# Performance work log

Hardware: AMD Instinct MI355X
Metric: run time of the kernel (lower is better)

Reference implementation:

```python
import jax, jax.numpy as jnp
import numpy as np

B, N = 1, 512
NODE_DIM, EDGE_DIM = 384, 128
H, SK, SV, PK, PV = 8, 16, 16, 4, 4
EPS = 1e-8
LN_EPS = 1e-5


def setup_inputs() -> dict:
    key = jax.random.key(0)
    ks = jax.random.split(key, 20)
    d, e = NODE_DIM, EDGE_DIM
    s = 0.02
    rn = lambda k, sh: jax.random.normal(k, sh, jnp.float32) * s
    # orthonormal per-residue rotations (valid rigid frames)
    R, _ = jnp.linalg.qr(jax.random.normal(ks[2], (B, N, 3, 3), jnp.float32))
    out_dim = H * (SV + EDGE_DIM + PV * 4)  # scalar + pairwise + points(3) + point norms(1)
    return dict(
        node_features=jax.random.normal(ks[0], (B, N, d), jnp.float32),
        edge_features=jax.random.normal(ks[1], (B, N, N, e), jnp.float32),
        rotations=R,
        translations=jax.random.normal(ks[3], (B, N, 3), jnp.float32),
        mask=jnp.ones((B, N), bool),
        Wq_s=rn(ks[4], (d, H * SK)), Wk_s=rn(ks[5], (d, H * SK)), Wv_s=rn(ks[6], (d, H * SV)),
        Wq_p=rn(ks[7], (d, H * PK * 3)), Wk_p=rn(ks[8], (d, H * PK * 3)), Wv_p=rn(ks[9], (d, H * PV * 3)),
        point_weights=jnp.full((H,), np.log(np.e - 1.0), jnp.float32),  # softplus -> 1
        Wb=rn(ks[10], (e, H)), bb=jnp.zeros((H,), jnp.float32),
        Wo=rn(ks[11], (out_dim, d)), bo=jnp.zeros((d,), jnp.float32),
        g1=jnp.ones((d,), jnp.float32), beta1=jnp.zeros((d,), jnp.float32),
        W1=rn(ks[12], (d, 2 * d)), b1=jnp.zeros((2 * d,), jnp.float32),
        W2=rn(ks[13], (2 * d, 2 * d)), b2=jnp.zeros((2 * d,), jnp.float32),
        W3=rn(ks[14], (2 * d, d)), b3=jnp.zeros((d,), jnp.float32),
        g2=jnp.ones((d,), jnp.float32), beta2=jnp.zeros((d,), jnp.float32),
    )


def _layer_norm(x, g, b):
    mu = x.mean(-1, keepdims=True)
    var = ((x - mu) ** 2).mean(-1, keepdims=True)
    return (x - mu) * jax.lax.rsqrt(var + LN_EPS) * g + b


def _forward(node_features, edge_features, rotations, translations, mask,
             Wq_s, Wk_s, Wv_s, Wq_p, Wk_p, Wv_p, point_weights, Wb, bb, Wo, bo,
             g1, beta1, W1, b1, W2, b2, W3, b3, g2, beta2):
    b, n, d = node_features.shape
    # num_attn_logits = 3 (scalar + point + pairwise)
    scal_scale = (3 * SK) ** -0.5
    point_scale = (3 * PK * 4.5) ** -0.5
    pair_scale = 3 ** -0.5

    qs = (node_features @ Wq_s).reshape(b, n, H, SK)
    kk = (node_features @ Wk_s).reshape(b, n, H, SK)
    vs = (node_features @ Wv_s).reshape(b, n, H, SV)

    def apply_rigid(p):  # p: (b,n,h,d,3); global = R^T applied per lucidrains einsum + t
        return jnp.einsum('bnhdc,bncr->bnhdr', p, rotations) + translations[:, :, None, None, :]

    qp = apply_rigid((node_features @ Wq_p).reshape(b, n, H, PK, 3))
    kp = apply_rigid((node_features @ Wk_p).reshape(b, n, H, PK, 3))
    vp = apply_rigid((node_features @ Wv_p).reshape(b, n, H, PV, 3))

    logits = jnp.einsum('bihk,bjhk->bhij', qs, kk) * scal_scale

    # point distance term: sum_{d,c} (q-k)^2 = |q|^2 + |k|^2 - 2 q.k (avoids (b,h,i,j,d,3) tensor)
    w = jax.nn.softplus(point_weights)  # (H,)
    q2 = jnp.einsum('bnhdc,bnhdc->bhn', qp, qp)
    k2 = jnp.einsum('bnhdc,bnhdc->bhn', kp, kp)
    cross = jnp.einsum('bihdc,bjhdc->bhij', qp, kp)
    dist = q2[..., :, None] + k2[..., None, :] - 2.0 * cross  # (b,h,i,j)
    logits = logits - 0.5 * point_scale * w[None, :, None, None] * dist

    pair_bias = (jnp.einsum('bije,eh->bhij', edge_features, Wb) + bb[None, :, None, None]) * pair_scale
    logits = logits + pair_bias

    pm = mask[:, None, :, None] & mask[:, None, None, :]  # (b,1,i,j)
    logits = jnp.where(pm, logits, -jnp.finfo(logits.dtype).max)
    attn = jax.nn.softmax(logits, axis=-1)  # (b,h,i,j)

    rs = jnp.einsum('bhij,bjhv->bihv', attn, vs).reshape(b, n, H * SV)
    rp = jnp.einsum('bhij,bije->bihe', attn, edge_features).reshape(b, n, H * EDGE_DIM)
    pts = jnp.einsum('bhij,bjhdc->bihdc', attn, vp)
    # invert rigid: subtract t, apply R (inverse of R^T application)
    local = jnp.einsum('bihdc,birc->bihdr', pts - translations[:, :, None, None, :], rotations)
    norms = jnp.sqrt((local ** 2).sum(-1) + EPS)  # (b,n,H,PV)

    cat = jnp.concatenate([rs, local.reshape(b, n, H * PV * 3), norms.reshape(b, n, H * PV), rp], axis=-1)
    ipa_out = cat @ Wo + bo

    x = _layer_norm(ipa_out, g1, beta1)  # dropout is identity at eval
    x = jax.nn.relu(x @ W1 + b1)
    x = jax.nn.relu(x @ W2 + b2)
    x = x @ W3 + b3
    return _layer_norm(x, g2, beta2)


def reference(node_features, edge_features, rotations, translations, mask,
              Wq_s, Wk_s, Wv_s, Wq_p, Wk_p, Wv_p, point_weights, Wb, bb, Wo, bo,
              g1, beta1, W1, b1, W2, b2, W3, b3, g2, beta2):
    return _forward(node_features, edge_features, rotations, translations, mask,
                    Wq_s, Wk_s, Wv_s, Wq_p, Wk_p, Wv_p, point_weights, Wb, bb, Wo, bo,
                    g1, beta1, W1, b1, W2, b2, W3, b3, g2, beta2)
```

## Files before the change

kernel.cpp:

```cpp
#include <hip/hip_runtime.h>
#include <cstddef>

#define NN 512
#define DD 384
#define EE 128
#define HH 8
#define JSPLIT 16

static constexpr float SCAL_SCALE  = 0.1443375673f;
static constexpr float POINT_SCALE = 0.1360827635f;
static constexpr float PAIR_SCALE  = 0.5773502692f;
static constexpr float LN_EPS = 1e-5f;
static constexpr float EPS    = 1e-8f;

typedef __bf16 bf16x8 __attribute__((ext_vector_type(8)));
typedef float  f32x4  __attribute__((ext_vector_type(4)));

__device__ __forceinline__ unsigned short bf16_bits(float v) {
    union { __bf16 b; unsigned short s; } c; c.b = (__bf16)v; return c.s;
}
__device__ __forceinline__ float bits2f(unsigned u) {
    union { unsigned u; float f; } c; c.u = u; return c.f;
}

__global__ __launch_bounds__(256) void prep_weights_kernel(
    const float* __restrict__ Wo, const float* __restrict__ W1,
    const float* __restrict__ W2, const float* __restrict__ W3,
    const float* __restrict__ Wq_s, const float* __restrict__ Wk_s,
    const float* __restrict__ Wv_s,
    const float* __restrict__ Wq_p, const float* __restrict__ Wk_p,
    const float* __restrict__ Wv_p, const float* __restrict__ nf,
    unsigned short* __restrict__ WoT, unsigned short* __restrict__ W1T,
    unsigned short* __restrict__ W2T, unsigned short* __restrict__ W3T,
    unsigned short* __restrict__ WprojT, unsigned short* __restrict__ nfb)
{
    const int b = blockIdx.x;
    if (b >= 1884) {
        const int idx = (b - 1884) * 1024 + threadIdx.x * 4;
        float4 v = *(const float4*)(nf + idx);
        unsigned lo = bf16_bits(v.x) | ((unsigned)bf16_bits(v.y) << 16);
        unsigned hi = bf16_bits(v.z) | ((unsigned)bf16_bits(v.w) << 16);
        uint2 pk; pk.x = lo; pk.y = hi;
        *(uint2*)(nfb + idx) = pk;
        return;
    }
    const float* W; unsigned short* out;
    int K, N, tile, rowoff = 0;
    if (b < 480)       { W = Wo;   out = WoT;    K = 1280; N = 384; tile = b; }
    else if (b < 768)  { W = W1;   out = W1T;    K = 384;  N = 768; tile = b - 480; }
    else if (b < 1344) { W = W2;   out = W2T;    K = 768;  N = 768; tile = b - 768; }
    else if (b < 1632) { W = W3;   out = W3T;    K = 768;  N = 384; tile = b - 1344; }
    else if (b < 1680) { W = Wq_s; out = WprojT; K = 384;  N = 128; tile = b - 1632; rowoff = 0; }
    else if (b < 1728) { W = Wk_s; out = WprojT; K = 384;  N = 128; tile = b - 1680; rowoff = 128; }
    else if (b < 1776) { W = Wv_s; out = WprojT; K = 384;  N = 128; tile = b - 1728; rowoff = 256; }
    else if (b < 1812) { W = Wq_p; out = WprojT; K = 384;  N = 96;  tile = b - 1776; rowoff = 384; }
    else if (b < 1848) { W = Wk_p; out = WprojT; K = 384;  N = 96;  tile = b - 1812; rowoff = 480; }
    else               { W = Wv_p; out = WprojT; K = 384;  N = 96;  tile = b - 1848; rowoff = 576; }

    const int ntn = N / 32;
    const int n0 = (tile % ntn) * 32, k0 = (tile / ntn) * 32;
    __shared__ float tb[32][33];
    const int tx = threadIdx.x & 31, ty = threadIdx.x >> 5;
    #pragma unroll
    for (int dy = 0; dy < 32; dy += 8)
        tb[ty + dy][tx] = W[(size_t)(k0 + ty + dy) * N + n0 + tx];
    __syncthreads();
    #pragma unroll
    for (int dy = 0; dy < 32; dy += 8)
        out[(size_t)(rowoff + n0 + ty + dy) * K + k0 + tx] = bf16_bits(tb[tx][ty + dy]);
}

__global__ __launch_bounds__(256) void edge_prep_kernel(
    const float* __restrict__ edge, const float* __restrict__ Wb,
    unsigned short* __restrict__ edgeT, float* __restrict__ biasG)
{
    const int bi = blockIdx.x;
    const int i = bi >> 2, jt = bi & 3;
    const int j0 = jt * 128;
    const int t = threadIdx.x;
    const int w = t >> 6, lane = t & 63, r = lane & 15, q = lane >> 4;

    __shared__ float ldsT[32][33];
    __shared__ unsigned short wbTl[16 * 128];

    if (t < 128) {
        float4 a = *(const float4*)&Wb[t * 8];
        float4 b = *(const float4*)&Wb[t * 8 + 4];
        wbTl[0 * 128 + t] = bf16_bits(a.x * PAIR_SCALE);
        wbTl[1 * 128 + t] = bf16_bits(a.y * PAIR_SCALE);
        wbTl[2 * 128 + t] = bf16_bits(a.z * PAIR_SCALE);
        wbTl[3 * 128 + t] = bf16_bits(a.w * PAIR_SCALE);
        wbTl[4 * 128 + t] = bf16_bits(b.x * PAIR_SCALE);
        wbTl[5 * 128 + t] = bf16_bits(b.y * PAIR_SCALE);
        wbTl[6 * 128 + t] = bf16_bits(b.z * PAIR_SCALE);
        wbTl[7 * 128 + t] = bf16_bits(b.w * PAIR_SCALE);
    } else {
        const int z = t - 128;
        #pragma unroll
        for (int s = 0; s < 8; s++) wbTl[1024 + z * 8 + s] = 0;
    }

    const float* etile = edge + ((size_t)i * 512 + j0) * 128;

    for (int sub = 0; sub < 16; sub++) {
        const int jb = (sub >> 2) * 32, eb = (sub & 3) * 32;
        __syncthreads();
        {
            const int jl = t >> 3, e4 = (t & 7) * 4;
            *(float4*)&ldsT[jl][e4] = *(const float4*)&etile[(size_t)(jb + jl) * 128 + eb + e4];
        }
        __syncthreads();
        if (t < 128) {
            const int e = t >> 2, jseg = (t & 3) * 8;
            union { uint4 u; unsigned short s[8]; } pk;
            #pragma unroll
            for (int s = 0; s < 8; s++) pk.s[s] = bf16_bits(ldsT[jseg + s][e]);
            *(uint4*)&edgeT[((size_t)i * 128 + eb + e) * 512 + j0 + jb + jseg] = pk.u;
        }
    }
    __syncthreads();

    #pragma unroll
    for (int rr = 0; rr < 2; rr++) {
        const int rt = w * 2 + rr;
        f32x4 acc = {0.f, 0.f, 0.f, 0.f};
        #pragma unroll
        for (int kk = 0; kk < 4; kk++) {
            const float* src = &etile[(size_t)(rt * 16 + r) * 128 + kk * 32 + q * 8];
            float4 f0 = *(const float4*)src;
            float4 f1 = *(const float4*)(src + 4);
            union { uint4 u; bf16x8 v; } aE;
            aE.u.x = (unsigned)bf16_bits(f0.x) | ((unsigned)bf16_bits(f0.y) << 16);
            aE.u.y = (unsigned)bf16_bits(f0.z) | ((unsigned)bf16_bits(f0.w) << 16);
            aE.u.z = (unsigned)bf16_bits(f1.x) | ((unsigned)bf16_bits(f1.y) << 16);
            aE.u.w = (unsigned)bf16_bits(f1.z) | ((unsigned)bf16_bits(f1.w) << 16);
            union { uint4 u; bf16x8 v; } bW;
            bW.u = *(const uint4*)&wbTl[r * 128 + kk * 32 + q * 8];
            acc = __builtin_amdgcn_mfma_f32_16x16x32_bf16(aE.v, bW.v, acc, 0, 0, 0);
        }
        if (r < 8)
            *(f32x4*)&biasG[((size_t)i * 8 + r) * 512 + j0 + rt * 16 + q * 4] = acc;
    }
}

template <int K, int NOUT, bool RELU, bool HASB, bool OUTBF>
__global__ __launch_bounds__(256) void gemm_bf16(
    const unsigned short* __restrict__ Xb, const unsigned short* __restrict__ Wt,
    const float* __restrict__ bias, void* __restrict__ Yv)
{
    const int t = threadIdx.x;
    const int w = t >> 6, lane = t & 63;
    const int r = lane & 15, q = lane >> 4;
    const int n0 = blockIdx.x * 16;
    const int m0 = blockIdx.y * 64 + w * 16;

    const unsigned short* xrow = Xb + (size_t)(m0 + r) * K + q * 8;
    const unsigned short* wrow = Wt + (size_t)(n0 + r) * K + q * 8;

    f32x4 acc = {0.f, 0.f, 0.f, 0.f};
    #pragma unroll 4
    for (int k0 = 0; k0 < K; k0 += 32) {
        union { uint4 u; bf16x8 v; } au, bu;
        au.u = *(const uint4*)(xrow + k0);
        bu.u = *(const uint4*)(wrow + k0);
        acc = __builtin_amdgcn_mfma_f32_16x16x32_bf16(au.v, bu.v, acc, 0, 0, 0);
    }
    const int n = n0 + r;
    const float bi = HASB ? bias[n] : 0.f;
    #pragma unroll
    for (int reg = 0; reg < 4; reg++) {
        const int m = m0 + q * 4 + reg;
        float v = acc[reg] + bi;
        if (RELU) v = fmaxf(v, 0.f);
        if (OUTBF) ((unsigned short*)Yv)[(size_t)m * NOUT + n] = bf16_bits(v);
        else       ((float*)Yv)[(size_t)m * NOUT + n] = v;
    }
}

__global__ __launch_bounds__(256) void ipa_post_kernel(
    const float* __restrict__ proj_out, const float* __restrict__ rot,
    const float* __restrict__ trans, const float* __restrict__ pw,
    const float* __restrict__ bb,
    unsigned short* __restrict__ Qp, unsigned short* __restrict__ Kp,
    unsigned short* __restrict__ svT)
{
    const int i = blockIdx.x;
    const int t = threadIdx.x;
    __shared__ float outs[672];
    __shared__ float ptg[288];
    __shared__ float q2s[8], k2s[8], pwh[8];

    for (int f = t; f < 672; f += 256) outs[f] = proj_out[(size_t)i * 672 + f];
    if (t < 8) pwh[t] = 0.5f * POINT_SCALE * log1pf(expf(pw[t]));
    __syncthreads();

    for (int f = t; f < 288; f += 256) {
        int which = f / 96, idx = f % 96;
        int hd = idx / 3, r = idx % 3;
        float acc = trans[(size_t)i * 3 + r];
        #pragma unroll
        for (int c = 0; c < 3; c++)
            acc += outs[384 + which * 96 + hd * 3 + c] * rot[(size_t)i * 9 + c * 3 + r];
        ptg[f] = acc;
    }
    __syncthreads();
    if (t < 16) {
        int which = t / 8, h = t % 8;
        float acc = 0.f;
        #pragma unroll
        for (int m = 0; m < 12; m++) {
            float v = ptg[which * 96 + h * 12 + m];
            acc += v * v;
        }
        (which ? k2s : q2s)[h] = acc;
    }
    __syncthreads();

    {
        const int h = t >> 5, d = t & 31;
        float qv, kv;
        if (d < 16)      { qv = outs[h * 16 + d] * SCAL_SCALE; kv = outs[128 + h * 16 + d]; }
        else if (d < 28) { qv = ptg[h * 12 + d - 16] * (2.f * pwh[h]); kv = ptg[96 + h * 12 + d - 16]; }
        else if (d == 28){ qv = -pwh[h] * q2s[h]; kv = 1.f; }
        else if (d == 29){ qv = 1.f; kv = -pwh[h] * k2s[h]; }
        else if (d == 30){ qv = 1.f; kv = bb[h] * PAIR_SCALE; }
        else             { qv = 0.f; kv = 0.f; }
        Qp[((size_t)i * 8 + h) * 32 + d] = bf16_bits(qv);
        Kp[((size_t)i * 8 + h) * 32 + d] = bf16_bits(kv);
    }
    if (t < 128) {
        int h = t >> 4, v = t & 15;
        svT[((size_t)h * 32 + v) * NN + i] = bf16_bits(outs[256 + h * 16 + v]);
    } else if (t < 224) {
        int idx = t - 128, h = idx / 12, m = idx % 12;
        svT[((size_t)h * 32 + 16 + m) * NN + i] = bf16_bits(ptg[192 + idx]);
    } else {
        int idx = t - 224;
        int h = idx >> 2, m = 28 + (idx & 3);
        svT[((size_t)h * 32 + m) * NN + i] = 0;
    }
}

__global__ __launch_bounds__(256) void ipa_fused2(
    const unsigned short* __restrict__ edgeT, const float* __restrict__ biasG,
    const unsigned short* __restrict__ Qp, const unsigned short* __restrict__ Kp,
    const unsigned short* __restrict__ svT,
    float* __restrict__ Opart, float* __restrict__ Mpart, float* __restrict__ Lpart)
{
    const int js = blockIdx.x;
    const int it = blockIdx.y;
    const int i0 = it * 8;
    const int jbase = js * 32;
    const int t = threadIdx.x;
    const int w = t >> 6, lane = t & 63;
    const int r = lane & 15, q = lane >> 4;

    __shared__ float Lqk[64 * 37];
    __shared__ __align__(16) unsigned short P1[8 * 16 * 32];
    __shared__ __align__(16) unsigned short P2[8 * 16 * 32];

    {
        uint4 z = {0u, 0u, 0u, 0u};
        uint4* p1 = (uint4*)P1; uint4* p2 = (uint4*)P2;
        for (int k = t; k < 512; k += 256) { p1[k] = z; p2[k] = z; }
    }

    #pragma unroll
    for (int hh = 0; hh < 2; hh++) {
        const int h = w * 2 + hh;
        bf16x8 aq = *(const bf16x8*)&Qp[((size_t)(i0 + (r & 7)) * 8 + h) * 32 + q * 8];
        #pragma unroll
        for (int jt = 0; jt < 2; jt++) {
            bf16x8 bk = *(const bf16x8*)&Kp[((size_t)(jbase + jt * 16 + r) * 8 + h) * 32 + q * 8];
            f32x4 acc = {0.f, 0.f, 0.f, 0.f};
            acc = __builtin_amdgcn_mfma_f32_16x16x32_bf16(aq, bk, acc, 0, 0, 0);
            if (q < 2) {
                #pragma unroll
                for (int reg = 0; reg < 4; reg++)
                    Lqk[(h * 8 + q * 4 + reg) * 37 + jt * 16 + r] = acc[reg];
            }
        }
    }
    __syncthreads();

    if (t < 64) {
        const int h = t >> 3, i = t & 7;
        const float* brow = biasG + ((size_t)(i0 + i) * 8 + h) * 512 + jbase;
        float lg[32];
        float mx = -1e30f;
        #pragma unroll
        for (int j = 0; j < 32; j++) {
            lg[j] = Lqk[t * 37 + j] + brow[j];
            mx = fmaxf(mx, lg[j]);
        }
        float sum = 0.f;
        #pragma unroll
        for (int j = 0; j < 32; j++) { lg[j] = __expf(lg[j] - mx); sum += lg[j]; }
        Mpart[(size_t)(js * 64 + it) * 64 + t] = mx;
        Lpart[(size_t)(js * 64 + it) * 64 + t] = sum;
        unsigned pk[16];
        #pragma unroll
        for (int s = 0; s < 16; s++)
            pk[s] = (unsigned)bf16_bits(lg[2 * s]) | ((unsigned)bf16_bits(lg[2 * s + 1]) << 16);
        uint4* d1 = (uint4*)&P1[((size_t)i * 16 + h) * 32];
        uint4* d2 = (uint4*)&P2[((size_t)h * 16 + i) * 32];
        #pragma unroll
        for (int s = 0; s < 4; s++) {
            uint4 v; v.x = pk[4*s]; v.y = pk[4*s+1]; v.z = pk[4*s+2]; v.w = pk[4*s+3];
            d1[s] = v; d2[s] = v;
        }
    }
    __syncthreads();

    #pragma unroll
    for (int ii = 0; ii < 2; ii++) {
        const int il = w * 2 + ii;
        const unsigned short* eT = edgeT + ((size_t)(i0 + il) * 128) * 512 + jbase;
        union { uint4 u; bf16x8 v; } bP;
        bP.u = *(const uint4*)&P1[((size_t)il * 16 + r) * 32 + q * 8];
        union { uint4 u; bf16x8 v; } aF[8];
        #pragma unroll
        for (int eb = 0; eb < 8; eb++)
            aF[eb].u = *(const uint4*)&eT[(size_t)(eb * 16 + r) * 512 + q * 8];
        f32x4 acc[8];
        #pragma unroll
        for (int eb = 0; eb < 8; eb++) {
            f32x4 c = {0.f, 0.f, 0.f, 0.f};
            acc[eb] = __builtin_amdgcn_mfma_f32_16x16x32_bf16(aF[eb].v, bP.v, c, 0, 0, 0);
        }
        float* orw = Opart + (size_t)((js * 64 + it) * 8 + il) * 1248;
        if (r < 8) {
            #pragma unroll
            for (int eb = 0; eb < 8; eb++)
                *(f32x4*)&orw[r * 156 + 28 + eb * 16 + q * 4] = acc[eb];
        }
    }

    #pragma unroll
    for (int hh = 0; hh < 2; hh++) {
        const int h = w * 2 + hh;
        union { uint4 u; bf16x8 v; } aP;
        aP.u = *(const uint4*)&P2[((size_t)h * 16 + r) * 32 + q * 8];
        #pragma unroll
        for (int ct = 0; ct < 2; ct++) {
            union { uint4 u; bf16x8 v; } bS;
            bS.u = *(const uint4*)&svT[((size_t)h * 32 + ct * 16 + r) * 512 + jbase + q * 8];
            f32x4 c = {0.f, 0.f, 0.f, 0.f};
            f32x4 acc = __builtin_amdgcn_mfma_f32_16x16x32_bf16(aP.v, bS.v, c, 0, 0, 0);
            const int cc = ct * 16 + r;
            if (q < 2 && cc < 28) {
                #pragma unroll
                for (int reg = 0; reg < 4; reg++) {
                    const int i = q * 4 + reg;
                    Opart[((size_t)((js * 64 + it) * 8 + i)) * 1248 + h * 156 + cc] = acc[reg];
                }
            }
        }
    }
}

__global__ __launch_bounds__(256) void ipa_merge(
    const float* __restrict__ Opart, const float* __restrict__ Mpart,
    const float* __restrict__ Lpart, const float* __restrict__ rot,
    const float* __restrict__ trans, unsigned short* __restrict__ cat_bf)
{
    const int i = blockIdx.x;
    const int itile = i >> 3, il = i & 7;
    const int t = threadIdx.x;
    __shared__ float wn[8 * JSPLIT];
    __shared__ float pts_s[96];

    if (t < 8) {
        const int h = t;
        float ms[JSPLIT], ls[JSPLIT], M = -1e30f;
        #pragma unroll
        for (int s = 0; s < JSPLIT; s++) {
            ms[s] = Mpart[(size_t)(s * 64 + itile) * 64 + h * 8 + il];
            ls[s] = Lpart[(size_t)(s * 64 + itile) * 64 + h * 8 + il];
            M = fmaxf(M, ms[s]);
        }
        float denom = 0.f, e[JSPLIT];
        #pragma unroll
        for (int s = 0; s < JSPLIT; s++) { e[s] = __expf(ms[s] - M); denom += e[s] * ls[s]; }
        const float inv = 1.f / denom;
        #pragma unroll
        for (int s = 0; s < JSPLIT; s++) wn[h * JSPLIT + s] = e[s] * inv;
    }
    __syncthreads();

    for (int col = t; col < 1248; col += 256) {
        const int h = col / 156, c = col % 156;
        float acc = 0.f;
        #pragma unroll
        for (int s = 0; s < JSPLIT; s++)
            acc += wn[h * JSPLIT + s] *
                   Opart[((size_t)(s * 64 + itile) * 8 + il) * 1248 + col];
        if (c < 16)      cat_bf[(size_t)i * 1280 + h * 16 + c] = bf16_bits(acc);
        else if (c < 28) pts_s[h * 12 + (c - 16)] = acc;
        else             cat_bf[(size_t)i * 1280 + 256 + h * 128 + (c - 28)] = bf16_bits(acc);
    }
    __syncthreads();

    const float* tr = trans + (size_t)i * 3;
    const float* R  = rot + (size_t)i * 9;
    if (t < 96) {
        int hd = t / 3, rr = t % 3;
        float acc = 0.f;
        #pragma unroll
        for (int c = 0; c < 3; c++)
            acc += (pts_s[hd * 3 + c] - tr[c]) * R[rr * 3 + c];
        cat_bf[(size_t)i * 1280 + 128 + t] = bf16_bits(acc);
    } else if (t < 128) {
        int pv = t - 96;
        float s = EPS;
        #pragma unroll
        for (int rr = 0; rr < 3; rr++) {
            float v = 0.f;
            #pragma unroll
            for (int c = 0; c < 3; c++)
                v += (pts_s[pv * 3 + c] - tr[c]) * R[rr * 3 + c];
            s += v * v;
        }
        cat_bf[(size_t)i * 1280 + 224 + pv] = bf16_bits(sqrtf(s));
    }
}

template <bool OUTBF>
__global__ __launch_bounds__(256) void ln_kernel(
    const float* __restrict__ X, const float* __restrict__ g,
    const float* __restrict__ beta, void* __restrict__ Yv, int Dim)
{
    __shared__ float red[4];
    __shared__ float bc;
    const int i = blockIdx.x;
    const int t = threadIdx.x;
    const float* x = X + (size_t)i * Dim;

    float s = 0.f;
    for (int k = t; k < Dim; k += 256) s += x[k];
    #pragma unroll
    for (int off = 32; off; off >>= 1) s += __shfl_down(s, off, 64);
    if ((t & 63) == 0) red[t >> 6] = s;
    __syncthreads();
    if (t == 0) bc = red[0] + red[1] + red[2] + red[3];
    __syncthreads();
    const float mu = bc / Dim;

    float v = 0.f;
    for (int k = t; k < Dim; k += 256) { float d = x[k] - mu; v += d * d; }
    #pragma unroll
    for (int off = 32; off; off >>= 1) v += __shfl_down(v, off, 64);
    __syncthreads();
    if ((t & 63) == 0) red[t >> 6] = v;
    __syncthreads();
    if (t == 0) bc = red[0] + red[1] + red[2] + red[3];
    __syncthreads();
    const float rstd = rsqrtf(bc / Dim + LN_EPS);

    for (int k = t; k < Dim; k += 256) {
        float val = (x[k] - mu) * rstd * g[k] + beta[k];
        if (OUTBF) ((unsigned short*)Yv)[(size_t)i * Dim + k] = bf16_bits(val);
        else       ((float*)Yv)[(size_t)i * Dim + k] = val;
    }
}

extern "C" void kernel_launch(void* const* d_in, const int* in_sizes, int n_in,
                              void* d_out, int out_size, void* d_ws, size_t ws_size,
                              hipStream_t stream)
{
    const float* nf    = (const float*)d_in[0];
    const float* edge  = (const float*)d_in[1];
    const float* rot   = (const float*)d_in[2];
    const float* trans = (const float*)d_in[3];
    const float* Wq_s = (const float*)d_in[5];
    const float* Wk_s = (const float*)d_in[6];
    const float* Wv_s = (const float*)d_in[7];
    const float* Wq_p = (const float*)d_in[8];
    const float* Wk_p = (const float*)d_in[9];
    const float* Wv_p = (const float*)d_in[10];
    const float* pw   = (const float*)d_in[11];
    const float* Wb   = (const float*)d_in[12];
    const float* bb   = (const float*)d_in[13];
    const float* Wo   = (const float*)d_in[14];
    const float* bo   = (const float*)d_in[15];
    const float* g1   = (const float*)d_in[16];
    const float* be1  = (const float*)d_in[17];
    const float* W1   = (const float*)d_in[18];
    const float* b1   = (const float*)d_in[19];
    const float* W2   = (const float*)d_in[20];
    const float* b2   = (const float*)d_in[21];
    const float* W3   = (const float*)d_in[22];
    const float* b3   = (const float*)d_in[23];
    const float* g2   = (const float*)d_in[24];
    const float* be2  = (const float*)d_in[25];

    float* ws = (float*)d_ws;
    float* proj_out = ws;
    float* ipa   = proj_out + 344064;
    float* y     = ipa + 196608;
    float* Opart = y + 196608;
    float* Mpart = Opart + 10223616;
    float* Lpart = Mpart + 65536;
    unsigned short* cat_bf = (unsigned short*)(Lpart + 65536);
    unsigned short* x1b = cat_bf + 655360;
    unsigned short* h1b = x1b + 196608;
    unsigned short* h2b = h1b + 393216;
    unsigned short* Qp  = h2b + 393216;
    unsigned short* Kp  = Qp + 131072;
    unsigned short* svT = Kp + 131072;
    unsigned short* WoT = svT + 131072;
    unsigned short* W1T = WoT + 491520;
    unsigned short* W2T = W1T + 294912;
    unsigned short* W3T = W2T + 589824;
    unsigned short* WprojT = W3T + 294912;
    unsigned short* nfb = WprojT + 258048;
    unsigned short* edgeT = nfb + 196608;
    float* biasG = (float*)(edgeT + 33554432);

    edge_prep_kernel<<<2048, 256, 0, stream>>>(edge, Wb, edgeT, biasG);

    prep_weights_kernel<<<2076, 256, 0, stream>>>(Wo, W1, W2, W3,
                                                  Wq_s, Wk_s, Wv_s, Wq_p, Wk_p, Wv_p, nf,
                                                  WoT, W1T, W2T, W3T, WprojT, nfb);

    gemm_bf16<384, 672, false, false, false><<<dim3(42, 8), 256, 0, stream>>>(nfb, WprojT, nullptr, proj_out);

    ipa_post_kernel<<<NN, 256, 0, stream>>>(proj_out, rot, trans, pw, bb, Qp, Kp, svT);

    ipa_fused2<<<dim3(JSPLIT, 64), 256, 0, stream>>>(edgeT, biasG, Qp, Kp, svT,
                                                     Opart, Mpart, Lpart);

    ipa_merge<<<NN, 256, 0, stream>>>(Opart, Mpart, Lpart, rot, trans, cat_bf);

    gemm_bf16<1280, 384, false, true, false><<<dim3(24, 8), 256, 0, stream>>>(cat_bf, WoT, bo, ipa);
    ln_kernel<true><<<NN, 256, 0, stream>>>(ipa, g1, be1, x1b, 384);

    gemm_bf16<384, 768, true, true, true><<<dim3(48, 8), 256, 0, stream>>>(x1b, W1T, b1, h1b);
    gemm_bf16<768, 768, true, true, true><<<dim3(48, 8), 256, 0, stream>>>(h1b, W2T, b2, h2b);
    gemm_bf16<768, 384, false, true, false><<<dim3(24, 8), 256, 0, stream>>>(h2b, W3T, b3, y);

    ln_kernel<false><<<NN, 256, 0, stream>>>(y, g2, be2, d_out, 384);
}
```

Measured before the change: 396.1 us.

## Retile transposed edge layout into per-j-split blocks and stage edge tile once

The edge prep kernel now processes a 32-row j-chunk per block, loading the full 32x128 fp32 edge tile into LDS once and reusing it both for the bf16 transpose and for the bias MFMA. The old version made 16 sync-separated sub-passes and then re-read the edge rows from global memory. The transposed edge buffer moves to a blocked [i][js][e][32] layout, so each attention block reads a contiguous 8KB chunk instead of rows strided by 512. The grid grows from 2048 to 8192 smaller blocks, and only half the waves do the bias MFMA.

```diff
diff --git a/kernel.cpp b/kernel.cpp
--- a/kernel.cpp
+++ b/kernel.cpp
@@ -75,12 +75,11 @@
     unsigned short* __restrict__ edgeT, float* __restrict__ biasG)
 {
     const int bi = blockIdx.x;
-    const int i = bi >> 2, jt = bi & 3;
-    const int j0 = jt * 128;
+    const int i = bi >> 4, js = bi & 15;
     const int t = threadIdx.x;
     const int w = t >> 6, lane = t & 63, r = lane & 15, q = lane >> 4;
 
-    __shared__ float ldsT[32][33];
+    __shared__ float ef[32][132];
     __shared__ unsigned short wbTl[16 * 128];
 
     if (t < 128) {
@@ -100,33 +99,39 @@
         for (int s = 0; s < 8; s++) wbTl[1024 + z * 8 + s] = 0;
     }
 
-    const float* etile = edge + ((size_t)i * 512 + j0) * 128;
-
-    for (int sub = 0; sub < 16; sub++) {
-        const int jb = (sub >> 2) * 32, eb = (sub & 3) * 32;
-        __syncthreads();
-        {
-            const int jl = t >> 3, e4 = (t & 7) * 4;
-            *(float4*)&ldsT[jl][e4] = *(const float4*)&etile[(size_t)(jb + jl) * 128 + eb + e4];
-        }
-        __syncthreads();
-        if (t < 128) {
-            const int e = t >> 2, jseg = (t & 3) * 8;
-            union { uint4 u; unsigned short s[8]; } pk;
-            #pragma unroll
-            for (int s = 0; s < 8; s++) pk.s[s] = bf16_bits(ldsT[jseg + s][e]);
-            *(uint4*)&edgeT[((size_t)i * 128 + eb + e) * 512 + j0 + jb + jseg] = pk.u;
-        }
-    }
-    __syncthreads();
-
-    #pragma unroll
-    for (int rr = 0; rr < 2; rr++) {
-        const int rt = w * 2 + rr;
+    const float* etile = edge + ((size_t)i * 512 + js * 32) * 128;
+    {
+        const int jl = t >> 3, base = (t & 7) * 16;
+        const float* src = etile + (size_t)jl * 128 + base;
+        float4 v0 = *(const float4*)(src + 0);
+        float4 v1 = *(const float4*)(src + 4);
+        float4 v2 = *(const float4*)(src + 8);
+        float4 v3 = *(const float4*)(src + 12);
+        *(float4*)&ef[jl][base + 0]  = v0;
+        *(float4*)&ef[jl][base + 4]  = v1;
+        *(float4*)&ef[jl][base + 8]  = v2;
+        *(float4*)&ef[jl][base + 12] = v3;
+    }
+    __syncthreads();
+
+    {
+        const int e = t & 127, jh = t >> 7;
+        union { uint4 u; unsigned short s[8]; } p0, p1;
+        #pragma unroll
+        for (int s = 0; s < 8; s++) p0.s[s] = bf16_bits(ef[jh * 16 + s][e]);
+        #pragma unroll
+        for (int s = 0; s < 8; s++) p1.s[s] = bf16_bits(ef[jh * 16 + 8 + s][e]);
+        unsigned short* dst = &edgeT[(((size_t)i * 16 + js) * 128 + e) * 32 + jh * 16];
+        *(uint4*)(dst + 0) = p0.u;
+        *(uint4*)(dst + 8) = p1.u;
+    }
+
+    if (w < 2) {
+        const int rt = w;
         f32x4 acc = {0.f, 0.f, 0.f, 0.f};
         #pragma unroll
         for (int kk = 0; kk < 4; kk++) {
-            const float* src = &etile[(size_t)(rt * 16 + r) * 128 + kk * 32 + q * 8];
+            const float* src = &ef[rt * 16 + r][kk * 32 + q * 8];
             float4 f0 = *(const float4*)src;
             float4 f1 = *(const float4*)(src + 4);
             union { uint4 u; bf16x8 v; } aE;
@@ -139,7 +144,7 @@
             acc = __builtin_amdgcn_mfma_f32_16x16x32_bf16(aE.v, bW.v, acc, 0, 0, 0);
         }
         if (r < 8)
-            *(f32x4*)&biasG[((size_t)i * 8 + r) * 512 + j0 + rt * 16 + q * 4] = acc;
+            *(f32x4*)&biasG[((size_t)i * 8 + r) * 512 + js * 32 + rt * 16 + q * 4] = acc;
     }
 }
 
@@ -315,13 +320,13 @@
     #pragma unroll
     for (int ii = 0; ii < 2; ii++) {
         const int il = w * 2 + ii;
-        const unsigned short* eT = edgeT + ((size_t)(i0 + il) * 128) * 512 + jbase;
+        const unsigned short* eT = edgeT + ((size_t)(i0 + il) * 16 + js) * 4096;
         union { uint4 u; bf16x8 v; } bP;
         bP.u = *(const uint4*)&P1[((size_t)il * 16 + r) * 32 + q * 8];
         union { uint4 u; bf16x8 v; } aF[8];
         #pragma unroll
         for (int eb = 0; eb < 8; eb++)
-            aF[eb].u = *(const uint4*)&eT[(size_t)(eb * 16 + r) * 512 + q * 8];
+            aF[eb].u = *(const uint4*)&eT[(eb * 16 + r) * 32 + q * 8];
         f32x4 acc[8];
         #pragma unroll
         for (int eb = 0; eb < 8; eb++) {
@@ -517,7 +522,7 @@
     unsigned short* edgeT = nfb + 196608;
     float* biasG = (float*)(edgeT + 33554432);
 
-    edge_prep_kernel<<<2048, 256, 0, stream>>>(edge, Wb, edgeT, biasG);
+    edge_prep_kernel<<<8192, 256, 0, stream>>>(edge, Wb, edgeT, biasG);
 
     prep_weights_kernel<<<2076, 256, 0, stream>>>(Wo, W1, W2, W3,
                                                   Wq_s, Wk_s, Wv_s, Wq_p, Wk_p, Wv_p, nf,
```

After: 353.8 us. 10.7% less time.

## Fuse edge transpose and pair-bias projection into the IPA attention kernel

Applied to the files above, without the earlier changes.

Removes the separate edge_prep kernel, which wrote a bf16 transposed copy of the full edge tensor plus a bias buffer to global memory. The attention kernel now reads fp32 edge features directly and computes the pair bias with MFMA. It also transposes each edge tile into LDS itself, processing 4 query rows at a time in two halves. This cuts a large intermediate write and read, at the cost of an uncoalesced strided gather of edge values and an extra fp32 edge read inside the main kernel.

```diff
diff --git a/kernel.cpp b/kernel.cpp
--- a/kernel.cpp
+++ b/kernel.cpp
@@ -70,79 +70,6 @@
         out[(size_t)(rowoff + n0 + ty + dy) * K + k0 + tx] = bf16_bits(tb[tx][ty + dy]);
 }
 
-__global__ __launch_bounds__(256) void edge_prep_kernel(
-    const float* __restrict__ edge, const float* __restrict__ Wb,
-    unsigned short* __restrict__ edgeT, float* __restrict__ biasG)
-{
-    const int bi = blockIdx.x;
-    const int i = bi >> 2, jt = bi & 3;
-    const int j0 = jt * 128;
-    const int t = threadIdx.x;
-    const int w = t >> 6, lane = t & 63, r = lane & 15, q = lane >> 4;
-
-    __shared__ float ldsT[32][33];
-    __shared__ unsigned short wbTl[16 * 128];
-
-    if (t < 128) {
-        float4 a = *(const float4*)&Wb[t * 8];
-        float4 b = *(const float4*)&Wb[t * 8 + 4];
-        wbTl[0 * 128 + t] = bf16_bits(a.x * PAIR_SCALE);
-        wbTl[1 * 128 + t] = bf16_bits(a.y * PAIR_SCALE);
-        wbTl[2 * 128 + t] = bf16_bits(a.z * PAIR_SCALE);
-        wbTl[3 * 128 + t] = bf16_bits(a.w * PAIR_SCALE);
-        wbTl[4 * 128 + t] = bf16_bits(b.x * PAIR_SCALE);
-        wbTl[5 * 128 + t] = bf16_bits(b.y * PAIR_SCALE);
-        wbTl[6 * 128 + t] = bf16_bits(b.z * PAIR_SCALE);
-        wbTl[7 * 128 + t] = bf16_bits(b.w * PAIR_SCALE);
-    } else {
-        const int z = t - 128;
-        #pragma unroll
-        for (int s = 0; s < 8; s++) wbTl[1024 + z * 8 + s] = 0;
-    }
-
-    const float* etile = edge + ((size_t)i * 512 + j0) * 128;
-
-    for (int sub = 0; sub < 16; sub++) {
-        const int jb = (sub >> 2) * 32, eb = (sub & 3) * 32;
-        __syncthreads();
-        {
-            const int jl = t >> 3, e4 = (t & 7) * 4;
-            *(float4*)&ldsT[jl][e4] = *(const float4*)&etile[(size_t)(jb + jl) * 128 + eb + e4];
-        }
-        __syncthreads();
-        if (t < 128) {
-            const int e = t >> 2, jseg = (t & 3) * 8;
-            union { uint4 u; unsigned short s[8]; } pk;
-            #pragma unroll
-            for (int s = 0; s < 8; s++) pk.s[s] = bf16_bits(ldsT[jseg + s][e]);
-            *(uint4*)&edgeT[((size_t)i * 128 + eb + e) * 512 + j0 + jb + jseg] = pk.u;
-        }
-    }
-    __syncthreads();
-
-    #pragma unroll
-    for (int rr = 0; rr < 2; rr++) {
-        const int rt = w * 2 + rr;
-        f32x4 acc = {0.f, 0.f, 0.f, 0.f};
-        #pragma unroll
-        for (int kk = 0; kk < 4; kk++) {
-            const float* src = &etile[(size_t)(rt * 16 + r) * 128 + kk * 32 + q * 8];
-            float4 f0 = *(const float4*)src;
-            float4 f1 = *(const float4*)(src + 4);
-            union { uint4 u; bf16x8 v; } aE;
-            aE.u.x = (unsigned)bf16_bits(f0.x) | ((unsigned)bf16_bits(f0.y) << 16);
-            aE.u.y = (unsigned)bf16_bits(f0.z) | ((unsigned)bf16_bits(f0.w) << 16);
-            aE.u.z = (unsigned)bf16_bits(f1.x) | ((unsigned)bf16_bits(f1.y) << 16);
-            aE.u.w = (unsigned)bf16_bits(f1.z) | ((unsigned)bf16_bits(f1.w) << 16);
-            union { uint4 u; bf16x8 v; } bW;
-            bW.u = *(const uint4*)&wbTl[r * 128 + kk * 32 + q * 8];
-            acc = __builtin_amdgcn_mfma_f32_16x16x32_bf16(aE.v, bW.v, acc, 0, 0, 0);
-        }
-        if (r < 8)
-            *(f32x4*)&biasG[((size_t)i * 8 + r) * 512 + j0 + rt * 16 + q * 4] = acc;
-    }
-}
-
 template <int K, int NOUT, bool RELU, bool HASB, bool OUTBF>
 __global__ __launch_bounds__(256) void gemm_bf16(
     const unsigned short* __restrict__ Xb, const unsigned short* __restrict__ Wt,
@@ -242,9 +169,9 @@
 }
 
 __global__ __launch_bounds__(256) void ipa_fused2(
-    const unsigned short* __restrict__ edgeT, const float* __restrict__ biasG,
+    const float* __restrict__ edge,
     const unsigned short* __restrict__ Qp, const unsigned short* __restrict__ Kp,
-    const unsigned short* __restrict__ svT,
+    const unsigned short* __restrict__ svT, const float* __restrict__ Wb,
     float* __restrict__ Opart, float* __restrict__ Mpart, float* __restrict__ Lpart)
 {
     const int js = blockIdx.x;
@@ -255,14 +182,23 @@
     const int w = t >> 6, lane = t & 63;
     const int r = lane & 15, q = lane >> 4;
 
-    __shared__ float Lqk[64 * 37];
-    __shared__ __align__(16) unsigned short P1[8 * 16 * 32];
-    __shared__ __align__(16) unsigned short P2[8 * 16 * 32];
-
-    {
-        uint4 z = {0u, 0u, 0u, 0u};
-        uint4* p1 = (uint4*)P1; uint4* p2 = (uint4*)P2;
-        for (int k = t; k < 512; k += 256) { p1[k] = z; p2[k] = z; }
+    __shared__ float Lqk[64 * 33];
+    __shared__ __align__(16) unsigned short P1[72 * 32];
+    __shared__ __align__(16) unsigned short P2[72 * 32];
+    __shared__ __align__(16) unsigned short wbTl[16 * 136];
+    __shared__ __align__(16) unsigned short eT[4 * 128 * 40];
+
+    if (t < 128) {
+        float4 a = *(const float4*)&Wb[t * 8];
+        float4 b = *(const float4*)&Wb[t * 8 + 4];
+        wbTl[0 * 136 + t] = bf16_bits(a.x * PAIR_SCALE);
+        wbTl[1 * 136 + t] = bf16_bits(a.y * PAIR_SCALE);
+        wbTl[2 * 136 + t] = bf16_bits(a.z * PAIR_SCALE);
+        wbTl[3 * 136 + t] = bf16_bits(a.w * PAIR_SCALE);
+        wbTl[4 * 136 + t] = bf16_bits(b.x * PAIR_SCALE);
+        wbTl[5 * 136 + t] = bf16_bits(b.y * PAIR_SCALE);
+        wbTl[6 * 136 + t] = bf16_bits(b.z * PAIR_SCALE);
+        wbTl[7 * 136 + t] = bf16_bits(b.w * PAIR_SCALE);
     }
 
     #pragma unroll
@@ -277,70 +213,116 @@
             if (q < 2) {
                 #pragma unroll
                 for (int reg = 0; reg < 4; reg++)
-                    Lqk[(h * 8 + q * 4 + reg) * 37 + jt * 16 + r] = acc[reg];
-            }
-        }
-    }
-    __syncthreads();
-
-    if (t < 64) {
-        const int h = t >> 3, i = t & 7;
-        const float* brow = biasG + ((size_t)(i0 + i) * 8 + h) * 512 + jbase;
-        float lg[32];
-        float mx = -1e30f;
-        #pragma unroll
-        for (int j = 0; j < 32; j++) {
-            lg[j] = Lqk[t * 37 + j] + brow[j];
-            mx = fmaxf(mx, lg[j]);
-        }
-        float sum = 0.f;
-        #pragma unroll
-        for (int j = 0; j < 32; j++) { lg[j] = __expf(lg[j] - mx); sum += lg[j]; }
-        Mpart[(size_t)(js * 64 + it) * 64 + t] = mx;
-        Lpart[(size_t)(js * 64 + it) * 64 + t] = sum;
-        unsigned pk[16];
-        #pragma unroll
-        for (int s = 0; s < 16; s++)
-            pk[s] = (unsigned)bf16_bits(lg[2 * s]) | ((unsigned)bf16_bits(lg[2 * s + 1]) << 16);
-        uint4* d1 = (uint4*)&P1[((size_t)i * 16 + h) * 32];
-        uint4* d2 = (uint4*)&P2[((size_t)h * 16 + i) * 32];
-        #pragma unroll
-        for (int s = 0; s < 4; s++) {
-            uint4 v; v.x = pk[4*s]; v.y = pk[4*s+1]; v.z = pk[4*s+2]; v.w = pk[4*s+3];
-            d1[s] = v; d2[s] = v;
-        }
-    }
-    __syncthreads();
-
-    #pragma unroll
-    for (int ii = 0; ii < 2; ii++) {
-        const int il = w * 2 + ii;
-        const unsigned short* eT = edgeT + ((size_t)(i0 + il) * 128) * 512 + jbase;
-        union { uint4 u; bf16x8 v; } bP;
-        bP.u = *(const uint4*)&P1[((size_t)il * 16 + r) * 32 + q * 8];
-        union { uint4 u; bf16x8 v; } aF[8];
-        #pragma unroll
-        for (int eb = 0; eb < 8; eb++)
-            aF[eb].u = *(const uint4*)&eT[(size_t)(eb * 16 + r) * 512 + q * 8];
-        f32x4 acc[8];
-        #pragma unroll
-        for (int eb = 0; eb < 8; eb++) {
-            f32x4 c = {0.f, 0.f, 0.f, 0.f};
-            acc[eb] = __builtin_amdgcn_mfma_f32_16x16x32_bf16(aF[eb].v, bP.v, c, 0, 0, 0);
-        }
-        float* orw = Opart + (size_t)((js * 64 + it) * 8 + il) * 1248;
-        if (r < 8) {
+                    Lqk[(h * 8 + q * 4 + reg) * 33 + jt * 16 + r] = acc[reg];
+            }
+        }
+    }
+    __syncthreads();
+
+    const int te = t >> 1, th8 = t & 1;
+
+    for (int half = 0; half < 2; half++) {
+        #pragma unroll
+        for (int k = 0; k < 4; k++) {
+            const int i = i0 + half * 4 + k;
+            const float* src = edge + ((size_t)i * 512 + jbase + th8 * 16) * 128 + te;
+            float v[16];
+            #pragma unroll
+            for (int s = 0; s < 16; s++) v[s] = src[(size_t)s * 128];
+            union { uint4 u2[2]; unsigned short sh[16]; } pk;
+            #pragma unroll
+            for (int s = 0; s < 16; s++) pk.sh[s] = bf16_bits(v[s]);
+            unsigned short* dst = &eT[k * 5120 + te * 40 + th8 * 16];
+            *(uint4*)(dst + 0) = pk.u2[0];
+            *(uint4*)(dst + 8) = pk.u2[1];
+        }
+        {
+            const int il = half * 4 + w;
+            const float* ebase = edge + ((size_t)(i0 + il) * 512 + jbase) * 128;
+            #pragma unroll
+            for (int jt = 0; jt < 2; jt++) {
+                f32x4 acc = {0.f, 0.f, 0.f, 0.f};
+                #pragma unroll
+                for (int kk = 0; kk < 4; kk++) {
+                    const float* srcb = ebase + (size_t)(jt * 16 + r) * 128 + kk * 32 + q * 8;
+                    float4 f0 = *(const float4*)srcb;
+                    float4 f1 = *(const float4*)(srcb + 4);
+                    union { uint4 u; bf16x8 v; } aE;
+                    aE.u.x = (unsigned)bf16_bits(f0.x) | ((unsigned)bf16_bits(f0.y) << 16);
+                    aE.u.y = (unsigned)bf16_bits(f0.z) | ((unsigned)bf16_bits(f0.w) << 16);
+                    aE.u.z = (unsigned)bf16_bits(f1.x) | ((unsigned)bf16_bits(f1.y) << 16);
+                    aE.u.w = (unsigned)bf16_bits(f1.z) | ((unsigned)bf16_bits(f1.w) << 16);
+                    union { uint4 u; bf16x8 v; } bW;
+                    bW.u = *(const uint4*)&wbTl[r * 136 + kk * 32 + q * 8];
+                    acc = __builtin_amdgcn_mfma_f32_16x16x32_bf16(aE.v, bW.v, acc, 0, 0, 0);
+                }
+                if (r < 8) {
+                    #pragma unroll
+                    for (int reg = 0; reg < 4; reg++)
+                        Lqk[(r * 8 + il) * 33 + jt * 16 + q * 4 + reg] += acc[reg];
+                }
+            }
+        }
+        __syncthreads();
+
+        if (t < 32) {
+            const int h = t >> 2, il = half * 4 + (t & 3);
+            const float* lrow = &Lqk[(h * 8 + il) * 33];
+            float lg[32];
+            float mx = -1e30f;
+            #pragma unroll
+            for (int j = 0; j < 32; j++) {
+                lg[j] = lrow[j];
+                mx = fmaxf(mx, lg[j]);
+            }
+            float sum = 0.f;
+            #pragma unroll
+            for (int j = 0; j < 32; j++) { lg[j] = __expf(lg[j] - mx); sum += lg[j]; }
+            Mpart[(size_t)(js * 64 + it) * 64 + h * 8 + il] = mx;
+            Lpart[(size_t)(js * 64 + it) * 64 + h * 8 + il] = sum;
+            unsigned pk[16];
+            #pragma unroll
+            for (int s = 0; s < 16; s++)
+                pk[s] = (unsigned)bf16_bits(lg[2 * s]) | ((unsigned)bf16_bits(lg[2 * s + 1]) << 16);
+            uint4* d1 = (uint4*)&P1[((size_t)il * 8 + h) * 32];
+            uint4* d2 = (uint4*)&P2[((size_t)h * 8 + il) * 32];
+            #pragma unroll
+            for (int s = 0; s < 4; s++) {
+                uint4 v; v.x = pk[4*s]; v.y = pk[4*s+1]; v.z = pk[4*s+2]; v.w = pk[4*s+3];
+                d1[s] = v; d2[s] = v;
+            }
+        }
+        __syncthreads();
+
+        {
+            const int il = half * 4 + w;
+            union { uint4 u; bf16x8 v; } bP;
+            bP.u = *(const uint4*)&P1[((size_t)il * 8 + r) * 32 + q * 8];
+            union { uint4 u; bf16x8 v; } aF[8];
             #pragma unroll
             for (int eb = 0; eb < 8; eb++)
-                *(f32x4*)&orw[r * 156 + 28 + eb * 16 + q * 4] = acc[eb];
-        }
+                aF[eb].u = *(const uint4*)&eT[w * 5120 + (eb * 16 + r) * 40 + q * 8];
+            f32x4 acc[8];
+            #pragma unroll
+            for (int eb = 0; eb < 8; eb++) {
+                f32x4 c = {0.f, 0.f, 0.f, 0.f};
+                acc[eb] = __builtin_amdgcn_mfma_f32_16x16x32_bf16(aF[eb].v, bP.v, c, 0, 0, 0);
+            }
+            float* orw = Opart + (size_t)((js * 64 + it) * 8 + il) * 1248;
+            if (r < 8) {
+                #pragma unroll
+                for (int eb = 0; eb < 8; eb++)
+                    *(f32x4*)&orw[r * 156 + 28 + eb * 16 + q * 4] = acc[eb];
+            }
+        }
+        __syncthreads();
     }
 
     #pragma unroll
     for (int hh = 0; hh < 2; hh++) {
         const int h = w * 2 + hh;
         union { uint4 u; bf16x8 v; } aP;
-        aP.u = *(const uint4*)&P2[((size_t)h * 16 + r) * 32 + q * 8];
+        aP.u = *(const uint4*)&P2[((size_t)h * 8 + r) * 32 + q * 8];
         #pragma unroll
         for (int ct = 0; ct < 2; ct++) {
             union { uint4 u; bf16x8 v; } bS;
@@ -514,10 +496,6 @@
     unsigned short* W3T = W2T + 589824;
     unsigned short* WprojT = W3T + 294912;
     unsigned short* nfb = WprojT + 258048;
-    unsigned short* edgeT = nfb + 196608;
-    float* biasG = (float*)(edgeT + 33554432);
-
-    edge_prep_kernel<<<2048, 256, 0, stream>>>(edge, Wb, edgeT, biasG);
 
     prep_weights_kernel<<<2076, 256, 0, stream>>>(Wo, W1, W2, W3,
                                                   Wq_s, Wk_s, Wv_s, Wq_p, Wk_p, Wv_p, nf,
@@ -527,7 +505,7 @@
 
     ipa_post_kernel<<<NN, 256, 0, stream>>>(proj_out, rot, trans, pw, bb, Qp, Kp, svT);
 
-    ipa_fused2<<<dim3(JSPLIT, 64), 256, 0, stream>>>(edgeT, biasG, Qp, Kp, svT,
+    ipa_fused2<<<dim3(JSPLIT, 64), 256, 0, stream>>>(edge, Qp, Kp, svT, Wb,
                                                      Opart, Mpart, Lpart);
 
     ipa_merge<<<NN, 256, 0, stream>>>(Opart, Mpart, Lpart, rot, trans, cat_bf);
```

New measurement: 335.6 us. 1.18x faster.
